# Optimization experiments

Hardware: AMD Instinct MI355X
Metric: run time of the kernel (lower is better)

Reference implementation:

```python
import jax, jax.numpy as jnp
import numpy as np

B, L, H_IN, N_FLOWS = 65536, 256, 300, 4


def householder(v, z):
    # z_new = z - 2 * v * (v . z) / ||v||^2   (fused; same math as vvT bmm chain)
    vz = jnp.sum(v * z, axis=1, keepdims=True)      # [B,1]
    norm_sq = jnp.sum(v * v, axis=1, keepdims=True)  # [B,1]
    return z - 2.0 * v * (vz / norm_sq)


def setup_inputs() -> dict:
    key = jax.random.key(0)
    ks = jax.random.split(key, 6)
    z = jax.random.normal(ks[0], (B, L), dtype=jnp.float32)
    h = jax.random.normal(ks[1], (B, H_IN), dtype=jnp.float32)
    W0 = jax.random.normal(ks[2], (L, H_IN), dtype=jnp.float32) * 0.05
    b0 = jax.random.normal(ks[3], (L,), dtype=jnp.float32) * 0.05
    Ws = jax.random.normal(ks[4], (N_FLOWS - 1, L, L), dtype=jnp.float32) * 0.05
    bs = jax.random.normal(ks[5], (N_FLOWS - 1, L), dtype=jnp.float32) * 0.05
    return {"z": z, "h": h, "W0": W0, "b0": b0, "Ws": Ws, "bs": bs}


def reference(z, h, W0, b0, Ws, bs):
    v = h @ W0.T + b0            # Linear(300 -> L)
    z = householder(v, z)
    for i in range(Ws.shape[0]):  # small fixed chain (n_flows-1)
        v = v @ Ws[i].T + bs[i]   # Linear(L -> L)
        z = householder(v, z)
    return z
```

## Files before the change

### kernel.cpp

```cpp
#include <hip/hip_runtime.h>

typedef __attribute__((ext_vector_type(4))) float f32x4;
typedef __attribute__((ext_vector_type(8))) short bf16x8;
typedef __attribute__((ext_vector_type(4))) unsigned int u32x4;
typedef unsigned short ushort_t;

#define B_ROWS 65536
#define L_DIM  256
#define H_IN_D 300
#define H_PAD  320
#define BM     64
#define LDH    328
#define LDV    264
#define NTH    256

__device__ __forceinline__ ushort_t f2bf(float f) {
  unsigned u = __builtin_bit_cast(unsigned, f);
  unsigned r = u + 0x7fffu + ((u >> 16) & 1u);
  return (ushort_t)(r >> 16);
}
__device__ __forceinline__ float bflo(unsigned u) { return __builtin_bit_cast(float, u << 16); }
__device__ __forceinline__ float bfhi(unsigned u) { return __builtin_bit_cast(float, u & 0xffff0000u); }

__global__ void cvt_w(const float* __restrict__ W0, const float* __restrict__ Ws,
                      ushort_t* __restrict__ W0b, ushort_t* __restrict__ Wsb) {
  int i = blockIdx.x * blockDim.x + threadIdx.x;
  int stride = gridDim.x * blockDim.x;
  for (int t = i; t < 256 * H_PAD; t += stride) {
    int n = t / H_PAD, k = t - n * H_PAD;
    W0b[t] = (k < H_IN_D) ? f2bf(W0[n * H_IN_D + k]) : (ushort_t)0;
  }
  for (int t = i; t < 3 * 256 * 256; t += stride) Wsb[t] = f2bf(Ws[t]);
}

template<int KSTEPS, int LDA>
__device__ __forceinline__ void gemm_stage(
    const ushort_t* __restrict__ Alds,
    const ushort_t* __restrict__ Bg, int ldb,
    const float* __restrict__ bias,
    ushort_t* __restrict__ Olds,
    int wave, int r, int g)
{
  f32x4 acc[4][4];
#pragma unroll
  for (int mt = 0; mt < 4; ++mt)
#pragma unroll
    for (int nt = 0; nt < 4; ++nt) { acc[mt][nt][0] = 0.f; acc[mt][nt][1] = 0.f; acc[mt][nt][2] = 0.f; acc[mt][nt][3] = 0.f; }

  const int c0 = wave * 64;
  const ushort_t* Abase = Alds + r * LDA + g * 8;
  const ushort_t* Bb0 = Bg + (c0 + 0 * 16 + r) * ldb + g * 8;
  const ushort_t* Bb1 = Bg + (c0 + 1 * 16 + r) * ldb + g * 8;
  const ushort_t* Bb2 = Bg + (c0 + 2 * 16 + r) * ldb + g * 8;
  const ushort_t* Bb3 = Bg + (c0 + 3 * 16 + r) * ldb + g * 8;

#pragma unroll
  for (int ks = 0; ks < KSTEPS; ++ks) {
    bf16x8 b0 = *(const bf16x8*)(Bb0 + ks * 32);
    bf16x8 b1 = *(const bf16x8*)(Bb1 + ks * 32);
    bf16x8 b2 = *(const bf16x8*)(Bb2 + ks * 32);
    bf16x8 b3 = *(const bf16x8*)(Bb3 + ks * 32);
    bf16x8 a[4];
#pragma unroll
    for (int mt = 0; mt < 4; ++mt) a[mt] = *(const bf16x8*)(Abase + mt * 16 * LDA + ks * 32);
#pragma unroll
    for (int mt = 0; mt < 4; ++mt) {
      acc[mt][0] = __builtin_amdgcn_mfma_f32_16x16x32_bf16(a[mt], b0, acc[mt][0], 0, 0, 0);
      acc[mt][1] = __builtin_amdgcn_mfma_f32_16x16x32_bf16(a[mt], b1, acc[mt][1], 0, 0, 0);
      acc[mt][2] = __builtin_amdgcn_mfma_f32_16x16x32_bf16(a[mt], b2, acc[mt][2], 0, 0, 0);
      acc[mt][3] = __builtin_amdgcn_mfma_f32_16x16x32_bf16(a[mt], b3, acc[mt][3], 0, 0, 0);
    }
  }

#pragma unroll
  for (int nt = 0; nt < 4; ++nt) {
    float bv = bias[c0 + nt * 16 + r];
#pragma unroll
    for (int mt = 0; mt < 4; ++mt) {
#pragma unroll
      for (int j = 0; j < 4; ++j) {
        float val = acc[mt][nt][j] + bv;
        Olds[(mt * 16 + g * 4 + j) * LDV + c0 + nt * 16 + r] = f2bf(val);
      }
    }
  }
}

__device__ __forceinline__ void dot_update(const ushort_t* __restrict__ V,
                                           int wave, int r, int g, float (&zr)[64])
{
  const ushort_t* vp = V + (wave * 16 + r) * LDV + g * 64;
  float vz = 0.f, vv = 0.f;
#pragma unroll
  for (int jb = 0; jb < 8; ++jb) {
    u32x4 q = *(const u32x4*)(vp + jb * 8);
#pragma unroll
    for (int w = 0; w < 4; ++w) {
      unsigned u = q[w];
      float f0 = bflo(u), f1 = bfhi(u);
      int i = jb * 8 + w * 2;
      vz = fmaf(f0, zr[i], vz);     vv = fmaf(f0, f0, vv);
      vz = fmaf(f1, zr[i + 1], vz); vv = fmaf(f1, f1, vv);
    }
  }
  vz += __shfl_xor(vz, 16); vz += __shfl_xor(vz, 32);
  vv += __shfl_xor(vv, 16); vv += __shfl_xor(vv, 32);
  float a = 2.f * vz / vv;
#pragma unroll
  for (int jb = 0; jb < 8; ++jb) {
    u32x4 q = *(const u32x4*)(vp + jb * 8);
#pragma unroll
    for (int w = 0; w < 4; ++w) {
      unsigned u = q[w];
      int i = jb * 8 + w * 2;
      zr[i]     = fmaf(-a, bflo(u), zr[i]);
      zr[i + 1] = fmaf(-a, bfhi(u), zr[i + 1]);
    }
  }
}

__global__ __launch_bounds__(NTH, 2) void flow_fused(
    const float* __restrict__ z, const float* __restrict__ h,
    const ushort_t* __restrict__ W0b, const float* __restrict__ b0,
    const ushort_t* __restrict__ Wsb, const float* __restrict__ bs,
    float* __restrict__ out)
{
  __shared__ __align__(16) ushort_t smem[BM * LDV + BM * LDH];
  ushort_t* vb0 = smem;
  ushort_t* vb1 = smem + BM * LDV;
  ushort_t* hbuf = vb1;

  const int tid  = threadIdx.x;
  const int wave = tid >> 6;
  const int lane = tid & 63;
  const int r    = lane & 15;
  const int g    = lane >> 4;
  const int row0 = blockIdx.x * BM;

  for (int row = wave; row < BM; row += 4) {
    const float* hrow = h + (row0 + row) * H_IN_D;
#pragma unroll
    for (int cc = 0; cc < 5; ++cc) {
      int c = lane + cc * 64;
      float v = (c < H_IN_D) ? hrow[c] : 0.f;
      hbuf[row * LDH + c] = f2bf(v);
    }
  }

  float zr[64];
  const int zrow = wave * 16 + r;
  {
    const float* zp = z + (row0 + zrow) * L_DIM + g * 64;
#pragma unroll
    for (int j = 0; j < 16; ++j) {
      f32x4 v = *(const f32x4*)(zp + j * 4);
      zr[j * 4 + 0] = v[0]; zr[j * 4 + 1] = v[1];
      zr[j * 4 + 2] = v[2]; zr[j * 4 + 3] = v[3];
    }
  }

  __syncthreads();

  gemm_stage<10, LDH>(hbuf, W0b, H_PAD, b0, vb0, wave, r, g);
  __syncthreads();
  dot_update(vb0, wave, r, g, zr);

  for (int s = 0; s < 3; ++s) {
    const ushort_t* src = (s & 1) ? vb1 : vb0;
    ushort_t*       dst = (s & 1) ? vb0 : vb1;
    gemm_stage<8, LDV>(src, Wsb + s * 256 * 256, 256, bs + s * 256, dst, wave, r, g);
    __syncthreads();
    dot_update(dst, wave, r, g, zr);
  }

  {
    float* op = out + (row0 + zrow) * L_DIM + g * 64;
#pragma unroll
    for (int j = 0; j < 16; ++j) {
      f32x4 v;
      v[0] = zr[j * 4 + 0]; v[1] = zr[j * 4 + 1];
      v[2] = zr[j * 4 + 2]; v[3] = zr[j * 4 + 3];
      *(f32x4*)(op + j * 4) = v;
    }
  }
}

extern "C" void kernel_launch(void* const* d_in, const int* in_sizes, int n_in,
                              void* d_out, int out_size, void* d_ws, size_t ws_size,
                              hipStream_t stream) {
  const float* z  = (const float*)d_in[0];
  const float* h  = (const float*)d_in[1];
  const float* W0 = (const float*)d_in[2];
  const float* b0 = (const float*)d_in[3];
  const float* Ws = (const float*)d_in[4];
  const float* bs = (const float*)d_in[5];
  float* out = (float*)d_out;

  ushort_t* W0b = (ushort_t*)d_ws;
  ushort_t* Wsb = W0b + 256 * H_PAD;

  hipLaunchKernelGGL(cvt_w, dim3(256), dim3(NTH), 0, stream, W0, Ws, W0b, Wsb);
  hipLaunchKernelGGL(flow_fused, dim3(B_ROWS / BM), dim3(NTH), 0, stream,
                     z, h, W0b, b0, Wsb, bs, out);
}
```

Before: 123.5 us.

## Halve row tile to 32 and raise occupancy with remapped Householder update

Cuts the per-block row tile from 64 to 32, which halves the MFMA accumulator and z register arrays, and raises launch bounds to 4 blocks per SIMD. The Householder dot-update is remapped so each row is spread over 8 lanes, with a 3-step shuffle reduction. Stages now ping-pong between the v buffer and the h buffer, each with its own leading dimension. The goal is more occupancy and latency hiding from smaller register and LDS footprints. The cost is that each block now reads the weights from global or L2 for half as many rows, doubling weight traffic per row.

```diff
diff --git a/kernel.cpp b/kernel.cpp
--- a/kernel.cpp
+++ b/kernel.cpp
@@ -9,7 +9,7 @@
 #define L_DIM  256
 #define H_IN_D 300
 #define H_PAD  320
-#define BM     64
+#define BM     32
 #define LDH    328
 #define LDV    264
 #define NTH    256
@@ -33,7 +33,7 @@
   for (int t = i; t < 3 * 256 * 256; t += stride) Wsb[t] = f2bf(Ws[t]);
 }
 
-template<int KSTEPS, int LDA>
+template<int KSTEPS, int LDA, int LDO>
 __device__ __forceinline__ void gemm_stage(
     const ushort_t* __restrict__ Alds,
     const ushort_t* __restrict__ Bg, int ldb,
@@ -41,34 +41,30 @@
     ushort_t* __restrict__ Olds,
     int wave, int r, int g)
 {
-  f32x4 acc[4][4];
-#pragma unroll
-  for (int mt = 0; mt < 4; ++mt)
+  f32x4 acc[2][4];
+#pragma unroll
+  for (int mt = 0; mt < 2; ++mt)
 #pragma unroll
     for (int nt = 0; nt < 4; ++nt) { acc[mt][nt][0] = 0.f; acc[mt][nt][1] = 0.f; acc[mt][nt][2] = 0.f; acc[mt][nt][3] = 0.f; }
 
   const int c0 = wave * 64;
   const ushort_t* Abase = Alds + r * LDA + g * 8;
-  const ushort_t* Bb0 = Bg + (c0 + 0 * 16 + r) * ldb + g * 8;
-  const ushort_t* Bb1 = Bg + (c0 + 1 * 16 + r) * ldb + g * 8;
-  const ushort_t* Bb2 = Bg + (c0 + 2 * 16 + r) * ldb + g * 8;
-  const ushort_t* Bb3 = Bg + (c0 + 3 * 16 + r) * ldb + g * 8;
+  const ushort_t* Bbase = Bg + (c0 + r) * ldb + g * 8;
 
 #pragma unroll
   for (int ks = 0; ks < KSTEPS; ++ks) {
-    bf16x8 b0 = *(const bf16x8*)(Bb0 + ks * 32);
-    bf16x8 b1 = *(const bf16x8*)(Bb1 + ks * 32);
-    bf16x8 b2 = *(const bf16x8*)(Bb2 + ks * 32);
-    bf16x8 b3 = *(const bf16x8*)(Bb3 + ks * 32);
-    bf16x8 a[4];
-#pragma unroll
-    for (int mt = 0; mt < 4; ++mt) a[mt] = *(const bf16x8*)(Abase + mt * 16 * LDA + ks * 32);
-#pragma unroll
-    for (int mt = 0; mt < 4; ++mt) {
-      acc[mt][0] = __builtin_amdgcn_mfma_f32_16x16x32_bf16(a[mt], b0, acc[mt][0], 0, 0, 0);
-      acc[mt][1] = __builtin_amdgcn_mfma_f32_16x16x32_bf16(a[mt], b1, acc[mt][1], 0, 0, 0);
-      acc[mt][2] = __builtin_amdgcn_mfma_f32_16x16x32_bf16(a[mt], b2, acc[mt][2], 0, 0, 0);
-      acc[mt][3] = __builtin_amdgcn_mfma_f32_16x16x32_bf16(a[mt], b3, acc[mt][3], 0, 0, 0);
+    bf16x8 b[4];
+#pragma unroll
+    for (int nt = 0; nt < 4; ++nt) b[nt] = *(const bf16x8*)(Bbase + nt * 16 * ldb + ks * 32);
+    bf16x8 a[2];
+#pragma unroll
+    for (int mt = 0; mt < 2; ++mt) a[mt] = *(const bf16x8*)(Abase + mt * 16 * LDA + ks * 32);
+#pragma unroll
+    for (int mt = 0; mt < 2; ++mt) {
+      acc[mt][0] = __builtin_amdgcn_mfma_f32_16x16x32_bf16(a[mt], b[0], acc[mt][0], 0, 0, 0);
+      acc[mt][1] = __builtin_amdgcn_mfma_f32_16x16x32_bf16(a[mt], b[1], acc[mt][1], 0, 0, 0);
+      acc[mt][2] = __builtin_amdgcn_mfma_f32_16x16x32_bf16(a[mt], b[2], acc[mt][2], 0, 0, 0);
+      acc[mt][3] = __builtin_amdgcn_mfma_f32_16x16x32_bf16(a[mt], b[3], acc[mt][3], 0, 0, 0);
     }
   }
 
@@ -76,23 +72,26 @@
   for (int nt = 0; nt < 4; ++nt) {
     float bv = bias[c0 + nt * 16 + r];
 #pragma unroll
-    for (int mt = 0; mt < 4; ++mt) {
+    for (int mt = 0; mt < 2; ++mt) {
 #pragma unroll
       for (int j = 0; j < 4; ++j) {
         float val = acc[mt][nt][j] + bv;
-        Olds[(mt * 16 + g * 4 + j) * LDV + c0 + nt * 16 + r] = f2bf(val);
+        Olds[(mt * 16 + g * 4 + j) * LDO + c0 + nt * 16 + r] = f2bf(val);
       }
     }
   }
 }
 
+template<int LDVx>
 __device__ __forceinline__ void dot_update(const ushort_t* __restrict__ V,
-                                           int wave, int r, int g, float (&zr)[64])
+                                           int wave, int lane, float (&zr)[32])
 {
-  const ushort_t* vp = V + (wave * 16 + r) * LDV + g * 64;
+  const int zrow = wave * 8 + (lane >> 3);
+  const int cb = (lane & 7) * 32;
+  const ushort_t* vp = V + zrow * LDVx + cb;
   float vz = 0.f, vv = 0.f;
 #pragma unroll
-  for (int jb = 0; jb < 8; ++jb) {
+  for (int jb = 0; jb < 4; ++jb) {
     u32x4 q = *(const u32x4*)(vp + jb * 8);
 #pragma unroll
     for (int w = 0; w < 4; ++w) {
@@ -103,11 +102,12 @@
       vz = fmaf(f1, zr[i + 1], vz); vv = fmaf(f1, f1, vv);
     }
   }
-  vz += __shfl_xor(vz, 16); vz += __shfl_xor(vz, 32);
-  vv += __shfl_xor(vv, 16); vv += __shfl_xor(vv, 32);
+  vz += __shfl_xor(vz, 1); vv += __shfl_xor(vv, 1);
+  vz += __shfl_xor(vz, 2); vv += __shfl_xor(vv, 2);
+  vz += __shfl_xor(vz, 4); vv += __shfl_xor(vv, 4);
   float a = 2.f * vz / vv;
 #pragma unroll
-  for (int jb = 0; jb < 8; ++jb) {
+  for (int jb = 0; jb < 4; ++jb) {
     u32x4 q = *(const u32x4*)(vp + jb * 8);
 #pragma unroll
     for (int w = 0; w < 4; ++w) {
@@ -119,16 +119,15 @@
   }
 }
 
-__global__ __launch_bounds__(NTH, 2) void flow_fused(
+__global__ __launch_bounds__(NTH, 4) void flow_fused(
     const float* __restrict__ z, const float* __restrict__ h,
     const ushort_t* __restrict__ W0b, const float* __restrict__ b0,
     const ushort_t* __restrict__ Wsb, const float* __restrict__ bs,
     float* __restrict__ out)
 {
   __shared__ __align__(16) ushort_t smem[BM * LDV + BM * LDH];
-  ushort_t* vb0 = smem;
-  ushort_t* vb1 = smem + BM * LDV;
-  ushort_t* hbuf = vb1;
+  ushort_t* vb0  = smem;
+  ushort_t* hbuf = smem + BM * LDV;
 
   const int tid  = threadIdx.x;
   const int wave = tid >> 6;
@@ -147,12 +146,13 @@
     }
   }
 
-  float zr[64];
-  const int zrow = wave * 16 + r;
+  float zr[32];
+  const int zrow = wave * 8 + (lane >> 3);
+  const int cb = (lane & 7) * 32;
   {
-    const float* zp = z + (row0 + zrow) * L_DIM + g * 64;
-#pragma unroll
-    for (int j = 0; j < 16; ++j) {
+    const float* zp = z + (row0 + zrow) * L_DIM + cb;
+#pragma unroll
+    for (int j = 0; j < 8; ++j) {
       f32x4 v = *(const f32x4*)(zp + j * 4);
       zr[j * 4 + 0] = v[0]; zr[j * 4 + 1] = v[1];
       zr[j * 4 + 2] = v[2]; zr[j * 4 + 3] = v[3];
@@ -161,22 +161,29 @@
 
   __syncthreads();
 
-  gemm_stage<10, LDH>(hbuf, W0b, H_PAD, b0, vb0, wave, r, g);
+  gemm_stage<10, LDH, LDV>(hbuf, W0b, H_PAD, b0, vb0, wave, r, g);
   __syncthreads();
-  dot_update(vb0, wave, r, g, zr);
-
+  dot_update<LDV>(vb0, wave, lane, zr);
+
+#pragma unroll
   for (int s = 0; s < 3; ++s) {
-    const ushort_t* src = (s & 1) ? vb1 : vb0;
-    ushort_t*       dst = (s & 1) ? vb0 : vb1;
-    gemm_stage<8, LDV>(src, Wsb + s * 256 * 256, 256, bs + s * 256, dst, wave, r, g);
-    __syncthreads();
-    dot_update(dst, wave, r, g, zr);
+    const ushort_t* Wp = Wsb + s * 256 * 256;
+    const float*    bp = bs + s * 256;
+    if ((s & 1) == 0) {
+      gemm_stage<8, LDV, LDH>(vb0, Wp, 256, bp, hbuf, wave, r, g);
+      __syncthreads();
+      dot_update<LDH>(hbuf, wave, lane, zr);
+    } else {
+      gemm_stage<8, LDH, LDV>(hbuf, Wp, 256, bp, vb0, wave, r, g);
+      __syncthreads();
+      dot_update<LDV>(vb0, wave, lane, zr);
+    }
   }
 
   {
-    float* op = out + (row0 + zrow) * L_DIM + g * 64;
-#pragma unroll
-    for (int j = 0; j < 16; ++j) {
+    float* op = out + (row0 + zrow) * L_DIM + cb;
+#pragma unroll
+    for (int j = 0; j < 8; ++j) {
       f32x4 v;
       v[0] = zr[j * 4 + 0]; v[1] = zr[j * 4 + 1];
       v[2] = zr[j * 4 + 2]; v[3] = zr[j * 4 + 3];
```

New measurement: 196.3 us. +58.9%, slower.

## Swap MFMA operand roles, single LDS buffer, vectorized bf16 epilogue and h load

Applied to the files above, without the earlier changes.

Swaps the MFMA operands so weights become the A operand and activations the B operand. Each lane's accumulator then holds 4 consecutive output columns, which lets the epilogue pack them and store 8-byte bf16 vectors to LDS instead of scalar 2-byte stores. The separate ping-pong buffers are merged into one LDS buffer reused in place, with an extra barrier per stage. This cuts LDS footprint, which may raise occupancy. The h staging now uses float4 loads packed to bf16 pairs, and the stage loop is unrolled.

```diff
diff --git a/kernel.cpp b/kernel.cpp
--- a/kernel.cpp
+++ b/kernel.cpp
@@ -2,6 +2,7 @@
 
 typedef __attribute__((ext_vector_type(4))) float f32x4;
 typedef __attribute__((ext_vector_type(8))) short bf16x8;
+typedef __attribute__((ext_vector_type(2))) unsigned int u32x2;
 typedef __attribute__((ext_vector_type(4))) unsigned int u32x4;
 typedef unsigned short ushort_t;
 
@@ -10,14 +11,16 @@
 #define H_IN_D 300
 #define H_PAD  320
 #define BM     64
-#define LDH    328
-#define LDV    264
+#define LDW    328
 #define NTH    256
 
 __device__ __forceinline__ ushort_t f2bf(float f) {
   unsigned u = __builtin_bit_cast(unsigned, f);
   unsigned r = u + 0x7fffu + ((u >> 16) & 1u);
   return (ushort_t)(r >> 16);
+}
+__device__ __forceinline__ unsigned pk2(float lo, float hi) {
+  return (unsigned)f2bf(lo) | ((unsigned)f2bf(hi) << 16);
 }
 __device__ __forceinline__ float bflo(unsigned u) { return __builtin_bit_cast(float, u << 16); }
 __device__ __forceinline__ float bfhi(unsigned u) { return __builtin_bit_cast(float, u & 0xffff0000u); }
@@ -33,55 +36,48 @@
   for (int t = i; t < 3 * 256 * 256; t += stride) Wsb[t] = f2bf(Ws[t]);
 }
 
-template<int KSTEPS, int LDA>
-__device__ __forceinline__ void gemm_stage(
-    const ushort_t* __restrict__ Alds,
-    const ushort_t* __restrict__ Bg, int ldb,
-    const float* __restrict__ bias,
-    ushort_t* __restrict__ Olds,
-    int wave, int r, int g)
-{
-  f32x4 acc[4][4];
-#pragma unroll
-  for (int mt = 0; mt < 4; ++mt)
-#pragma unroll
-    for (int nt = 0; nt < 4; ++nt) { acc[mt][nt][0] = 0.f; acc[mt][nt][1] = 0.f; acc[mt][nt][2] = 0.f; acc[mt][nt][3] = 0.f; }
-
-  const int c0 = wave * 64;
-  const ushort_t* Abase = Alds + r * LDA + g * 8;
-  const ushort_t* Bb0 = Bg + (c0 + 0 * 16 + r) * ldb + g * 8;
-  const ushort_t* Bb1 = Bg + (c0 + 1 * 16 + r) * ldb + g * 8;
-  const ushort_t* Bb2 = Bg + (c0 + 2 * 16 + r) * ldb + g * 8;
-  const ushort_t* Bb3 = Bg + (c0 + 3 * 16 + r) * ldb + g * 8;
-
+template<int KSTEPS>
+__device__ __forceinline__ void gemm_acc(
+    const ushort_t* __restrict__ Slds,
+    const ushort_t* __restrict__ Wg, int ldb,
+    int wave, int r, int g, f32x4 (&acc)[4][4])
+{
+  const ushort_t* xb = Wg + (wave * 64 + r) * ldb + g * 8;
+  const ushort_t* yb = Slds + r * LDW + g * 8;
 #pragma unroll
   for (int ks = 0; ks < KSTEPS; ++ks) {
-    bf16x8 b0 = *(const bf16x8*)(Bb0 + ks * 32);
-    bf16x8 b1 = *(const bf16x8*)(Bb1 + ks * 32);
-    bf16x8 b2 = *(const bf16x8*)(Bb2 + ks * 32);
-    bf16x8 b3 = *(const bf16x8*)(Bb3 + ks * 32);
-    bf16x8 a[4];
-#pragma unroll
-    for (int mt = 0; mt < 4; ++mt) a[mt] = *(const bf16x8*)(Abase + mt * 16 * LDA + ks * 32);
+    bf16x8 x[4];
+#pragma unroll
+    for (int nt = 0; nt < 4; ++nt) x[nt] = *(const bf16x8*)(xb + nt * 16 * ldb + ks * 32);
+    bf16x8 y[4];
+#pragma unroll
+    for (int mt = 0; mt < 4; ++mt) y[mt] = *(const bf16x8*)(yb + mt * 16 * LDW + ks * 32);
+#pragma unroll
+    for (int nt = 0; nt < 4; ++nt) {
+      acc[nt][0] = __builtin_amdgcn_mfma_f32_16x16x32_bf16(x[nt], y[0], acc[nt][0], 0, 0, 0);
+      acc[nt][1] = __builtin_amdgcn_mfma_f32_16x16x32_bf16(x[nt], y[1], acc[nt][1], 0, 0, 0);
+      acc[nt][2] = __builtin_amdgcn_mfma_f32_16x16x32_bf16(x[nt], y[2], acc[nt][2], 0, 0, 0);
+      acc[nt][3] = __builtin_amdgcn_mfma_f32_16x16x32_bf16(x[nt], y[3], acc[nt][3], 0, 0, 0);
+    }
+  }
+}
+
+__device__ __forceinline__ void epi_write(
+    f32x4 (&acc)[4][4], const float* __restrict__ bias,
+    ushort_t* __restrict__ Slds, int wave, int r, int g)
+{
+#pragma unroll
+  for (int nt = 0; nt < 4; ++nt) {
+    const int n0 = wave * 64 + nt * 16 + g * 4;
+    f32x4 bv = *(const f32x4*)(bias + n0);
 #pragma unroll
     for (int mt = 0; mt < 4; ++mt) {
-      acc[mt][0] = __builtin_amdgcn_mfma_f32_16x16x32_bf16(a[mt], b0, acc[mt][0], 0, 0, 0);
-      acc[mt][1] = __builtin_amdgcn_mfma_f32_16x16x32_bf16(a[mt], b1, acc[mt][1], 0, 0, 0);
-      acc[mt][2] = __builtin_amdgcn_mfma_f32_16x16x32_bf16(a[mt], b2, acc[mt][2], 0, 0, 0);
-      acc[mt][3] = __builtin_amdgcn_mfma_f32_16x16x32_bf16(a[mt], b3, acc[mt][3], 0, 0, 0);
-    }
-  }
-
-#pragma unroll
-  for (int nt = 0; nt < 4; ++nt) {
-    float bv = bias[c0 + nt * 16 + r];
-#pragma unroll
-    for (int mt = 0; mt < 4; ++mt) {
-#pragma unroll
-      for (int j = 0; j < 4; ++j) {
-        float val = acc[mt][nt][j] + bv;
-        Olds[(mt * 16 + g * 4 + j) * LDV + c0 + nt * 16 + r] = f2bf(val);
-      }
+      float v0 = acc[nt][mt][0] + bv[0];
+      float v1 = acc[nt][mt][1] + bv[1];
+      float v2 = acc[nt][mt][2] + bv[2];
+      float v3 = acc[nt][mt][3] + bv[3];
+      u32x2 p; p[0] = pk2(v0, v1); p[1] = pk2(v2, v3);
+      *(u32x2*)&Slds[(mt * 16 + r) * LDW + n0] = p;
     }
   }
 }
@@ -89,7 +85,7 @@
 __device__ __forceinline__ void dot_update(const ushort_t* __restrict__ V,
                                            int wave, int r, int g, float (&zr)[64])
 {
-  const ushort_t* vp = V + (wave * 16 + r) * LDV + g * 64;
+  const ushort_t* vp = V + (wave * 16 + r) * LDW + g * 64;
   float vz = 0.f, vv = 0.f;
 #pragma unroll
   for (int jb = 0; jb < 8; ++jb) {
@@ -103,8 +99,8 @@
       vz = fmaf(f1, zr[i + 1], vz); vv = fmaf(f1, f1, vv);
     }
   }
-  vz += __shfl_xor(vz, 16); vz += __shfl_xor(vz, 32);
-  vv += __shfl_xor(vv, 16); vv += __shfl_xor(vv, 32);
+  vz += __shfl_xor(vz, 16); vv += __shfl_xor(vv, 16);
+  vz += __shfl_xor(vz, 32); vv += __shfl_xor(vv, 32);
   float a = 2.f * vz / vv;
 #pragma unroll
   for (int jb = 0; jb < 8; ++jb) {
@@ -125,10 +121,7 @@
     const ushort_t* __restrict__ Wsb, const float* __restrict__ bs,
     float* __restrict__ out)
 {
-  __shared__ __align__(16) ushort_t smem[BM * LDV + BM * LDH];
-  ushort_t* vb0 = smem;
-  ushort_t* vb1 = smem + BM * LDV;
-  ushort_t* hbuf = vb1;
+  __shared__ __align__(16) ushort_t S[BM * LDW];
 
   const int tid  = threadIdx.x;
   const int wave = tid >> 6;
@@ -139,11 +132,14 @@
 
   for (int row = wave; row < BM; row += 4) {
     const float* hrow = h + (row0 + row) * H_IN_D;
-#pragma unroll
-    for (int cc = 0; cc < 5; ++cc) {
-      int c = lane + cc * 64;
-      float v = (c < H_IN_D) ? hrow[c] : 0.f;
-      hbuf[row * LDH + c] = f2bf(v);
+    f32x4 m4 = *(const f32x4*)(hrow + 4 * lane);
+    u32x2 pm; pm[0] = pk2(m4[0], m4[1]); pm[1] = pk2(m4[2], m4[3]);
+    *(u32x2*)&S[row * LDW + 4 * lane] = pm;
+    if (lane < 16) {
+      f32x4 t4 = {0.f, 0.f, 0.f, 0.f};
+      if (lane < 11) t4 = *(const f32x4*)(hrow + 256 + 4 * lane);
+      u32x2 pt; pt[0] = pk2(t4[0], t4[1]); pt[1] = pk2(t4[2], t4[3]);
+      *(u32x2*)&S[row * LDW + 256 + 4 * lane] = pt;
     }
   }
 
@@ -161,16 +157,31 @@
 
   __syncthreads();
 
-  gemm_stage<10, LDH>(hbuf, W0b, H_PAD, b0, vb0, wave, r, g);
+  {
+    f32x4 acc[4][4];
+#pragma unroll
+    for (int a = 0; a < 4; ++a)
+#pragma unroll
+      for (int b = 0; b < 4; ++b) { acc[a][b][0]=0.f; acc[a][b][1]=0.f; acc[a][b][2]=0.f; acc[a][b][3]=0.f; }
+    gemm_acc<10>(S, W0b, H_PAD, wave, r, g, acc);
+    __syncthreads();
+    epi_write(acc, b0, S, wave, r, g);
+  }
   __syncthreads();
-  dot_update(vb0, wave, r, g, zr);
-
+  dot_update(S, wave, r, g, zr);
+
+#pragma unroll
   for (int s = 0; s < 3; ++s) {
-    const ushort_t* src = (s & 1) ? vb1 : vb0;
-    ushort_t*       dst = (s & 1) ? vb0 : vb1;
-    gemm_stage<8, LDV>(src, Wsb + s * 256 * 256, 256, bs + s * 256, dst, wave, r, g);
+    f32x4 acc[4][4];
+#pragma unroll
+    for (int a = 0; a < 4; ++a)
+#pragma unroll
+      for (int b = 0; b < 4; ++b) { acc[a][b][0]=0.f; acc[a][b][1]=0.f; acc[a][b][2]=0.f; acc[a][b][3]=0.f; }
+    gemm_acc<8>(S, Wsb + s * 256 * 256, 256, wave, r, g, acc);
     __syncthreads();
-    dot_update(dst, wave, r, g, zr);
+    epi_write(acc, bs + s * 256, S, wave, r, g);
+    __syncthreads();
+    dot_update(S, wave, r, g, zr);
   }
 
   {
```

New measurement: 134.7 us. 1.09x slower.
